# Kernel tuning notes

Hardware: AMD Instinct MI355X
Metric: run time of the kernel (lower is better)

The kernel has to match this reference:

```python
import jax, jax.numpy as jnp
import numpy as np

N_NODES = 100000
N_EDGES = 1600000
D_IN = 64
D_OUT = 64
E_DIM = 32
N_NODE_TYPES = 2
N_EDGE_TYPES = 3


def setup_inputs() -> dict:
    key = jax.random.key(0)
    ks = jax.random.split(key, 7)
    node_feature = jax.random.normal(ks[0], (N_NODES, D_IN), dtype=jnp.float32)
    edge_feature = jax.random.normal(ks[1], (N_EDGES, E_DIM), dtype=jnp.float32)
    # linear_node[i]: Linear(din, dout, bias=False) -> stored as [in, out]
    W_node = jax.random.normal(ks[2], (N_NODE_TYPES, D_IN, D_OUT), dtype=jnp.float32) / np.sqrt(D_IN)
    # linear_msg[i]: Linear(dout + edge_dim, dout, bias=False), msg_direction='single'
    W_msg = jax.random.normal(ks[3], (N_EDGE_TYPES, D_OUT + E_DIM, D_OUT), dtype=jnp.float32) / np.sqrt(D_OUT + E_DIM)
    node_type = jax.random.randint(ks[4], (N_NODES,), 0, N_NODE_TYPES, dtype=jnp.int32)
    edge_type = jax.random.randint(ks[5], (N_EDGES,), 0, N_EDGE_TYPES, dtype=jnp.int32)
    edge_index = jax.random.randint(ks[6], (2, N_EDGES), 0, N_NODES, dtype=jnp.int32)
    return {
        "node_feature": node_feature,
        "edge_feature": edge_feature,
        "W_node": W_node,
        "W_msg": W_msg,
        "node_type": node_type,
        "edge_type": edge_type,
        "edge_index": edge_index,
    }


def reference(node_feature, edge_feature, W_node, W_msg, node_type, edge_type, edge_index):
    # Per-node-type linear: x_out[n] = x[n] @ W_node[node_type[n]]
    # (compute per type, select by mask -- equivalent to masked gather + index_add)
    x_out = jnp.zeros((node_feature.shape[0], W_node.shape[2]), dtype=node_feature.dtype)
    for t in range(W_node.shape[0]):
        x_out = x_out + jnp.where((node_type == t)[:, None],
                                  node_feature @ W_node[t], 0.0)

    src, dst = edge_index[0], edge_index[1]
    # msg_direction == 'single': concat(x_j, edge_feature)  [E, dout+edge_dim]
    x_cat = jnp.concatenate([x_out[src], edge_feature], axis=-1)
    # Per-edge-type linear on messages
    msg = jnp.zeros((x_cat.shape[0], W_msg.shape[2]), dtype=x_cat.dtype)
    for t in range(W_msg.shape[0]):
        msg = msg + jnp.where((edge_type == t)[:, None], x_cat @ W_msg[t], 0.0)

    # normalize_adj=False -> norm is None; aggr='add' scatter into target nodes
    out = jax.ops.segment_sum(msg, dst, num_segments=node_feature.shape[0])
    return out
```

## Files before the change

### kernel.cpp

```cpp
#include <hip/hip_runtime.h>
#include <hip/hip_bf16.h>

#define N_NODES 100000
#define N_EDGES 1600000
#define D_IN 64
#define D_OUT 64
#define E_DIM 32
#define KCAT 288
#define NK (4 * N_NODES)
#define NBCHUNK 391

typedef unsigned long long u64;
typedef __hip_bfloat16 bf16;
typedef unsigned char u8;

__device__ __forceinline__ float bflo(unsigned u) {
    union { unsigned v; float f; } x; x.v = u << 16; return x.f;
}
__device__ __forceinline__ float bfhi(unsigned u) {
    union { unsigned v; float f; } x; x.v = u & 0xffff0000u; return x.f;
}
__device__ __forceinline__ unsigned packbf2(float a, float b) {
    union { bf16 h[2]; unsigned u; } w;
    w.h[0] = __float2bfloat16(a); w.h[1] = __float2bfloat16(b);
    return w.u;
}

__global__ __launch_bounds__(256) void zero_buf(float4* __restrict__ p, long n4) {
    long i = (long)blockIdx.x * 256 + threadIdx.x;
    long stride = (long)gridDim.x * 256;
    float4 z = make_float4(0.f, 0.f, 0.f, 0.f);
    for (; i < n4; i += stride) p[i] = z;
}

__global__ __launch_bounds__(256) void node_xform_g(const float* __restrict__ nf,
                                                    const float* __restrict__ Wn,
                                                    const int* __restrict__ ntype,
                                                    bf16* __restrict__ xout) {
    __shared__ float Ws[2 * 64 * 64];
    __shared__ float As[64][65];
    int tid = threadIdx.x;
    int n0 = blockIdx.x * 64;
    for (int i = tid; i < 2 * 64 * 64; i += 256) Ws[i] = Wn[i];
#pragma unroll
    for (int i = 0; i < 4; ++i) {
        int f = (i * 256 + tid) * 4;
        int r = f >> 6, c = f & 63;
        int n = n0 + r;
        float4 v = (n < N_NODES) ? *(const float4*)&nf[(size_t)n * 64 + c]
                                 : make_float4(0.f, 0.f, 0.f, 0.f);
        As[r][c + 0] = v.x; As[r][c + 1] = v.y; As[r][c + 2] = v.z; As[r][c + 3] = v.w;
    }
    __syncthreads();
    int tx = tid & 15, ty = tid >> 4;
    int r0 = n0 + ty * 4;
    int t0 = (r0 + 0 < N_NODES) ? ntype[r0 + 0] : 0;
    int t1 = (r0 + 1 < N_NODES) ? ntype[r0 + 1] : 0;
    int t2 = (r0 + 2 < N_NODES) ? ntype[r0 + 2] : 0;
    int t3 = (r0 + 3 < N_NODES) ? ntype[r0 + 3] : 0;
    float4 acc0 = {0,0,0,0}, acc1 = {0,0,0,0}, acc2 = {0,0,0,0}, acc3 = {0,0,0,0};
#pragma unroll 8
    for (int k = 0; k < 64; ++k) {
        float4 w0 = *(const float4*)&Ws[k * 64 + tx * 4];
        float4 w1 = *(const float4*)&Ws[4096 + k * 64 + tx * 4];
        float a0 = As[ty * 4 + 0][k];
        float a1 = As[ty * 4 + 1][k];
        float a2 = As[ty * 4 + 2][k];
        float a3 = As[ty * 4 + 3][k];
        float4 wa = t0 ? w1 : w0;
        float4 wb = t1 ? w1 : w0;
        float4 wc = t2 ? w1 : w0;
        float4 wd = t3 ? w1 : w0;
        acc0.x = fmaf(a0, wa.x, acc0.x); acc0.y = fmaf(a0, wa.y, acc0.y);
        acc0.z = fmaf(a0, wa.z, acc0.z); acc0.w = fmaf(a0, wa.w, acc0.w);
        acc1.x = fmaf(a1, wb.x, acc1.x); acc1.y = fmaf(a1, wb.y, acc1.y);
        acc1.z = fmaf(a1, wb.z, acc1.z); acc1.w = fmaf(a1, wb.w, acc1.w);
        acc2.x = fmaf(a2, wc.x, acc2.x); acc2.y = fmaf(a2, wc.y, acc2.y);
        acc2.z = fmaf(a2, wc.z, acc2.z); acc2.w = fmaf(a2, wc.w, acc2.w);
        acc3.x = fmaf(a3, wd.x, acc3.x); acc3.y = fmaf(a3, wd.y, acc3.y);
        acc3.z = fmaf(a3, wd.z, acc3.z); acc3.w = fmaf(a3, wd.w, acc3.w);
    }
#pragma unroll
    for (int r = 0; r < 4; ++r) {
        int n = r0 + r;
        if (n < N_NODES) {
            float4 a = (r == 0) ? acc0 : (r == 1) ? acc1 : (r == 2) ? acc2 : acc3;
            union { bf16 h[4]; uint2 u; } pk;
            pk.h[0] = __float2bfloat16(a.x); pk.h[1] = __float2bfloat16(a.y);
            pk.h[2] = __float2bfloat16(a.z); pk.h[3] = __float2bfloat16(a.w);
            *(uint2*)&xout[(size_t)n * 64 + tx * 4] = pk.u;
        }
    }
}

__global__ __launch_bounds__(256) void count_rank(const int* __restrict__ eidx,
                                                  const int* __restrict__ etype,
                                                  int* __restrict__ cnt,
                                                  u8* __restrict__ rank) {
    int i = blockIdx.x * 256 + threadIdx.x;
    if (i >= N_EDGES / 4) return;
    int4 d = ((const int4*)(eidx + N_EDGES))[i];
    int4 t = ((const int4*)etype)[i];
    int r0 = atomicAdd(&cnt[4 * d.x + t.x], 1);
    int r1 = atomicAdd(&cnt[4 * d.y + t.y], 1);
    int r2 = atomicAdd(&cnt[4 * d.z + t.z], 1);
    int r3 = atomicAdd(&cnt[4 * d.w + t.w], 1);
    ((uchar4*)rank)[i] = make_uchar4((u8)r0, (u8)r1, (u8)r2, (u8)r3);
}

__global__ __launch_bounds__(256) void scan_a(const int* __restrict__ cnt,
                                              int* __restrict__ partials) {
    __shared__ int ws[4];
    int b = blockIdx.x, tid = threadIdx.x, lane = tid & 63, wid = tid >> 6;
    int i0 = b * 1024 + tid * 4;
    int s = 0;
#pragma unroll
    for (int k = 0; k < 4; ++k) { int i = i0 + k; if (i < NK) s += cnt[i]; }
#pragma unroll
    for (int d = 32; d > 0; d >>= 1) s += __shfl_down(s, d);
    if (lane == 0) ws[wid] = s;
    __syncthreads();
    if (tid == 0) partials[b] = ws[0] + ws[1] + ws[2] + ws[3];
}

__global__ __launch_bounds__(512) void scan_b(int* __restrict__ partials) {
    __shared__ int s[512];
    int tid = threadIdx.x;
    int v = (tid < NBCHUNK) ? partials[tid] : 0;
    s[tid] = v;
    __syncthreads();
    for (int d = 1; d < 512; d <<= 1) {
        int u = (tid >= d) ? s[tid - d] : 0;
        __syncthreads();
        s[tid] += u;
        __syncthreads();
    }
    if (tid < NBCHUNK) partials[tid] = s[tid] - v;
}

__global__ __launch_bounds__(256) void scan_c(const int* __restrict__ cnt,
                                              const int* __restrict__ partials,
                                              int* __restrict__ offs) {
    __shared__ int wsum[4];
    int b = blockIdx.x, tid = threadIdx.x, lane = tid & 63, wid = tid >> 6;
    int i0 = b * 1024 + tid * 4;
    int c0 = (i0 + 0 < NK) ? cnt[i0 + 0] : 0;
    int c1 = (i0 + 1 < NK) ? cnt[i0 + 1] : 0;
    int c2 = (i0 + 2 < NK) ? cnt[i0 + 2] : 0;
    int c3 = (i0 + 3 < NK) ? cnt[i0 + 3] : 0;
    int lsum = c0 + c1 + c2 + c3;
    int v = lsum;
#pragma unroll
    for (int d = 1; d < 64; d <<= 1) {
        int u = __shfl_up(v, d);
        if (lane >= d) v += u;
    }
    int wexcl = v - lsum;
    if (lane == 63) wsum[wid] = v;
    __syncthreads();
    int bexcl = 0;
    for (int w = 0; w < wid; ++w) bexcl += wsum[w];
    int base = partials[b] + bexcl + wexcl;
    if (i0 + 0 < NK) offs[i0 + 0] = base; base += c0;
    if (i0 + 1 < NK) offs[i0 + 1] = base; base += c1;
    if (i0 + 2 < NK) offs[i0 + 2] = base; base += c2;
    if (i0 + 3 < NK) offs[i0 + 3] = base;
}

__global__ __launch_bounds__(256) void place_pay(const int* __restrict__ eidx,
                                                 const int* __restrict__ etype,
                                                 const u8* __restrict__ rank,
                                                 const int* __restrict__ offs,
                                                 u64* __restrict__ pay) {
    int i = blockIdx.x * 256 + threadIdx.x;
    if (i >= N_EDGES) return;
    int d = eidx[N_EDGES + i];
    int s = eidx[i];
    int t = etype[i];
    int pos = offs[4 * d + t] + (int)rank[i];
    pay[pos] = (u64)(unsigned)s | ((u64)(unsigned)i << 32);
}

__global__ __launch_bounds__(256) void aggregate_g(const u64* __restrict__ pay,
                                                   const int* __restrict__ offs,
                                                   const bf16* __restrict__ xout,
                                                   const float* __restrict__ ef,
                                                   bf16* __restrict__ B) {
    int wid = threadIdx.x >> 6, lane = threadIdx.x & 63;
    int gw = blockIdx.x * 4 + wid, nw = gridDim.x * 4;
    int c = lane & 31, half = lane >> 5;
    const unsigned short* xo = (const unsigned short*)xout;
    if (gw >= N_NODES) return;

    int4 o = ((const int4*)offs)[gw];
    for (int n = gw; n < N_NODES; n += nw) {
        int nn = n + nw;
        int4 onext;
        if (nn < N_NODES) onext = ((const int4*)offs)[nn];
        int beg = __builtin_amdgcn_readfirstlane(o.x);
        int y   = __builtin_amdgcn_readfirstlane(o.y);
        int z   = __builtin_amdgcn_readfirstlane(o.z);
        int end = __builtin_amdgcn_readfirstlane(o.w);
        float xa0 = 0.f, xa1 = 0.f, xb0 = 0.f, xb1 = 0.f, xc0 = 0.f, xc1 = 0.f;
        float ea = 0.f, eb = 0.f, ec = 0.f;

        for (int base = beg; base < end; base += 64) {
            int m = end - base; if (m > 64) m = 64;
            u64 p = (lane < m) ? pay[base + lane] : 0ull;
            int plo = (int)(unsigned)p;
            int phi = (int)(unsigned)(p >> 32);
            for (int j = 0; j < m; j += 16) {
                int sgp[8], egp[8];
#pragma unroll
                for (int q = 0; q < 8; ++q) {
                    int a  = __builtin_amdgcn_readlane(plo, j + 2 * q);
                    int b2 = __builtin_amdgcn_readlane(plo, j + 2 * q + 1);
                    sgp[q] = half ? b2 : a;
                    a  = __builtin_amdgcn_readlane(phi, j + 2 * q);
                    b2 = __builtin_amdgcn_readlane(phi, j + 2 * q + 1);
                    egp[q] = half ? b2 : a;
                }
                unsigned xv[8];
                float evv[8];
#pragma unroll
                for (int q = 0; q < 8; ++q) {
                    xv[q]  = *(const unsigned*)(xo + (size_t)sgp[q] * 64 + c * 2);
                    evv[q] = ef[(size_t)egp[q] * 32 + c];
                }
#pragma unroll
                for (int q = 0; q < 8; ++q) {
                    float xl = bflo(xv[q]), xh = bfhi(xv[q]);
                    float ev = evv[q];
                    int i0 = base + j + 2 * q;
                    if (i0 + 1 < y) {
                        xa0 += xl; xa1 += xh; ea += ev;
                    } else if (i0 >= y && i0 + 1 < z) {
                        xb0 += xl; xb1 += xh; eb += ev;
                    } else if (i0 >= z && i0 + 1 < end) {
                        xc0 += xl; xc1 += xh; ec += ev;
                    } else {
                        int idx = i0 + half;
                        bool v = idx < end;
                        float fl = v ? xl : 0.f, fh = v ? xh : 0.f, fe = v ? ev : 0.f;
                        if (idx < y)      { xa0 += fl; xa1 += fh; ea += fe; }
                        else if (idx < z) { xb0 += fl; xb1 += fh; eb += fe; }
                        else              { xc0 += fl; xc1 += fh; ec += fe; }
                    }
                }
            }
        }
        xa0 += __shfl_down(xa0, 32); xa1 += __shfl_down(xa1, 32);
        xb0 += __shfl_down(xb0, 32); xb1 += __shfl_down(xb1, 32);
        xc0 += __shfl_down(xc0, 32); xc1 += __shfl_down(xc1, 32);
        ea  += __shfl_down(ea, 32);  eb  += __shfl_down(eb, 32);  ec += __shfl_down(ec, 32);

        if (lane < 32) {
            bf16* Bn = B + (size_t)n * KCAT;
            *(unsigned*)&Bn[2 * c]       = packbf2(xa0, xa1);
            *(unsigned*)&Bn[64 + 2 * c]  = packbf2(xb0, xb1);
            *(unsigned*)&Bn[128 + 2 * c] = packbf2(xc0, xc1);
            Bn[192 + c] = __float2bfloat16(ea);
            Bn[224 + c] = __float2bfloat16(eb);
            Bn[256 + c] = __float2bfloat16(ec);
        }
        o = onext;
    }
}

__global__ __launch_bounds__(256) void final_gemm(const bf16* __restrict__ B,
                                                  const float* __restrict__ Wm,
                                                  float* __restrict__ out) {
    __shared__ float As[64][36];
    __shared__ float Ws[32][64];
    int tid = threadIdx.x;
    int n0 = blockIdx.x * 64;
    int tx = tid & 15;
    int ty = tid >> 4;
    float acc[4][4] = {};

    for (int k0 = 0; k0 < KCAT; k0 += 32) {
        {
            int r = tid >> 2, cb = (tid & 3) * 8;
            int n = n0 + r;
            uint4 v = make_uint4(0u, 0u, 0u, 0u);
            if (n < N_NODES) v = *(const uint4*)&B[(size_t)n * KCAT + k0 + cb];
            *(float4*)&As[r][cb]     = make_float4(bflo(v.x), bfhi(v.x), bflo(v.y), bfhi(v.y));
            *(float4*)&As[r][cb + 4] = make_float4(bflo(v.z), bfhi(v.z), bflo(v.w), bfhi(v.w));
        }
#pragma unroll
        for (int i = 0; i < 2; ++i) {
            int f = (i * 256 + tid) * 4;
            int kk = f >> 6, j = f & 63;
            int r = k0 + kk;
            int t, kin;
            if (r < 192) { t = r >> 6; kin = r & 63; }
            else         { int q = r - 192; t = q >> 5; kin = 64 + (q & 31); }
            *(float4*)&Ws[kk][j] = *(const float4*)&Wm[(t * 96 + kin) * 64 + j];
        }
        __syncthreads();
#pragma unroll
        for (int kk = 0; kk < 32; ++kk) {
            float a0 = As[ty * 4 + 0][kk];
            float a1 = As[ty * 4 + 1][kk];
            float a2 = As[ty * 4 + 2][kk];
            float a3 = As[ty * 4 + 3][kk];
            float4 w = *(const float4*)&Ws[kk][tx * 4];
            acc[0][0] = fmaf(a0, w.x, acc[0][0]); acc[0][1] = fmaf(a0, w.y, acc[0][1]);
            acc[0][2] = fmaf(a0, w.z, acc[0][2]); acc[0][3] = fmaf(a0, w.w, acc[0][3]);
            acc[1][0] = fmaf(a1, w.x, acc[1][0]); acc[1][1] = fmaf(a1, w.y, acc[1][1]);
            acc[1][2] = fmaf(a1, w.z, acc[1][2]); acc[1][3] = fmaf(a1, w.w, acc[1][3]);
            acc[2][0] = fmaf(a2, w.x, acc[2][0]); acc[2][1] = fmaf(a2, w.y, acc[2][1]);
            acc[2][2] = fmaf(a2, w.z, acc[2][2]); acc[2][3] = fmaf(a2, w.w, acc[2][3]);
            acc[3][0] = fmaf(a3, w.x, acc[3][0]); acc[3][1] = fmaf(a3, w.y, acc[3][1]);
            acc[3][2] = fmaf(a3, w.z, acc[3][2]); acc[3][3] = fmaf(a3, w.w, acc[3][3]);
        }
        __syncthreads();
    }
#pragma unroll
    for (int r = 0; r < 4; ++r) {
        int n = n0 + ty * 4 + r;
        if (n < N_NODES) {
            float4 v = make_float4(acc[r][0], acc[r][1], acc[r][2], acc[r][3]);
            *(float4*)&out[(size_t)n * 64 + tx * 4] = v;
        }
    }
}

__global__ __launch_bounds__(256) void fallback_edge(const float* __restrict__ nf,
                                                     const float* __restrict__ ef,
                                                     const float* __restrict__ Wn,
                                                     const float* __restrict__ Wm,
                                                     const int* __restrict__ ntype,
                                                     const int* __restrict__ etype,
                                                     const int* __restrict__ eidx,
                                                     float* __restrict__ out) {
    __shared__ float wn[2 * 64 * 64];
    __shared__ float wm[3 * 96 * 64];
    for (int i = threadIdx.x; i < 2 * 64 * 64; i += 256) wn[i] = Wn[i];
    for (int i = threadIdx.x; i < 3 * 96 * 64; i += 256) wm[i] = Wm[i];
    __syncthreads();
    int wid = threadIdx.x >> 6, lane = threadIdx.x & 63;
    for (int e = blockIdx.x * 4 + wid; e < N_EDGES; e += gridDim.x * 4) {
        int t = etype[e];
        int s = eidx[e];
        int d = eidx[N_EDGES + e];
        int nt = ntype[s];
        float xs = nf[(long)s * 64 + lane];
        const float* wcol = &wn[nt * 4096 + lane];
        float xo = 0.f;
#pragma unroll 16
        for (int k = 0; k < 64; ++k) xo = fmaf(__shfl(xs, k), wcol[k * 64], xo);
        float ev = ef[(long)e * 32 + (lane & 31)];
        const float* mcol = &wm[t * 96 * 64 + lane];
        float m = 0.f;
#pragma unroll 16
        for (int k = 0; k < 64; ++k) m = fmaf(__shfl(xo, k), mcol[k * 64], m);
#pragma unroll 8
        for (int k = 0; k < 32; ++k) m = fmaf(__shfl(ev, k), mcol[(64 + k) * 64], m);
        atomicAdd(&out[(long)d * 64 + lane], m);
    }
}

extern "C" void kernel_launch(void* const* d_in, const int* in_sizes, int n_in,
                              void* d_out, int out_size, void* d_ws, size_t ws_size,
                              hipStream_t stream) {
    const float* nf    = (const float*)d_in[0];
    const float* ef    = (const float*)d_in[1];
    const float* Wn    = (const float*)d_in[2];
    const float* Wm    = (const float*)d_in[3];
    const int*   ntype = (const int*)d_in[4];
    const int*   etype = (const int*)d_in[5];
    const int*   eidx  = (const int*)d_in[6];
    float* out = (float*)d_out;

    const size_t xout_bytes = (size_t)N_NODES * 64 * 2;
    const size_t b_bytes    = (size_t)N_NODES * KCAT * 2;

    if (ws_size >= xout_bytes + b_bytes) {
        bf16* xout = (bf16*)d_ws;
        bf16* B    = (bf16*)((char*)d_ws + xout_bytes);
        u64* pay      = (u64*)d_out;
        int* cnt      = (int*)(pay + N_EDGES);
        int* offs     = cnt + NK;
        int* partials = offs + NK;
        u8*  rank     = (u8*)(partials + 512);

        zero_buf<<<400, 256, 0, stream>>>((float4*)cnt, (long)(NK / 4));
        node_xform_g<<<(N_NODES + 63) / 64, 256, 0, stream>>>(nf, Wn, ntype, xout);
        count_rank<<<(N_EDGES / 4 + 255) / 256, 256, 0, stream>>>(eidx, etype, cnt, rank);
        scan_a<<<NBCHUNK, 256, 0, stream>>>(cnt, partials);
        scan_b<<<1, 512, 0, stream>>>(partials);
        scan_c<<<NBCHUNK, 256, 0, stream>>>(cnt, partials, offs);
        place_pay<<<(N_EDGES + 255) / 256, 256, 0, stream>>>(eidx, etype, rank, offs, pay);
        aggregate_g<<<4096, 256, 0, stream>>>(pay, offs, xout, ef, B);
        final_gemm<<<(N_NODES + 63) / 64, 256, 0, stream>>>(B, Wm, out);
    } else {
        zero_buf<<<2048, 256, 0, stream>>>((float4*)d_out, (long)((size_t)out_size * 4 / 16));
        fallback_edge<<<4096, 256, 0, stream>>>(nf, ef, Wn, Wm, ntype, etype, eidx, out);
    }
}
```

Baseline: 310.6 us.

## Fuse count zeroing into node transform and prefetch next node's payload in aggregation

Removes the separate zero_buf launch by zeroing the count array inside node_xform_g. count_rank is switched to one edge per thread with scalar loads. aggregate_g now loads the first payload chunk of the next node while processing the current node, to hide memory latency. The single-edge count_rank loses int4 vectorized loads and adds more threads.

```diff
diff --git a/kernel.cpp b/kernel.cpp
--- a/kernel.cpp
+++ b/kernel.cpp
@@ -36,11 +36,16 @@
 __global__ __launch_bounds__(256) void node_xform_g(const float* __restrict__ nf,
                                                     const float* __restrict__ Wn,
                                                     const int* __restrict__ ntype,
-                                                    bf16* __restrict__ xout) {
+                                                    bf16* __restrict__ xout,
+                                                    int* __restrict__ cnt) {
     __shared__ float Ws[2 * 64 * 64];
     __shared__ float As[64][65];
     int tid = threadIdx.x;
     int n0 = blockIdx.x * 64;
+    {
+        int zi = blockIdx.x * 256 + tid;
+        if (zi < NK) cnt[zi] = 0;
+    }
     for (int i = tid; i < 2 * 64 * 64; i += 256) Ws[i] = Wn[i];
 #pragma unroll
     for (int i = 0; i < 4; ++i) {
@@ -98,14 +103,11 @@
                                                   int* __restrict__ cnt,
                                                   u8* __restrict__ rank) {
     int i = blockIdx.x * 256 + threadIdx.x;
-    if (i >= N_EDGES / 4) return;
-    int4 d = ((const int4*)(eidx + N_EDGES))[i];
-    int4 t = ((const int4*)etype)[i];
-    int r0 = atomicAdd(&cnt[4 * d.x + t.x], 1);
-    int r1 = atomicAdd(&cnt[4 * d.y + t.y], 1);
-    int r2 = atomicAdd(&cnt[4 * d.z + t.z], 1);
-    int r3 = atomicAdd(&cnt[4 * d.w + t.w], 1);
-    ((uchar4*)rank)[i] = make_uchar4((u8)r0, (u8)r1, (u8)r2, (u8)r3);
+    if (i >= N_EDGES) return;
+    int d = eidx[N_EDGES + i];
+    int t = etype[i];
+    int r = atomicAdd(&cnt[4 * d + t], 1);
+    rank[i] = (u8)r;
 }
 
 __global__ __launch_bounds__(256) void scan_a(const int* __restrict__ cnt,
@@ -193,10 +195,28 @@
     if (gw >= N_NODES) return;
 
     int4 o = ((const int4*)offs)[gw];
+    {
+        int b0 = __builtin_amdgcn_readfirstlane(o.x);
+        int e0 = __builtin_amdgcn_readfirstlane(o.w);
+        (void)b0; (void)e0;
+    }
+    u64 p = 0ull;
+    {
+        int beg = __builtin_amdgcn_readfirstlane(o.x);
+        int end = __builtin_amdgcn_readfirstlane(o.w);
+        if (beg + lane < end) p = pay[beg + lane];
+    }
+
     for (int n = gw; n < N_NODES; n += nw) {
         int nn = n + nw;
-        int4 onext;
-        if (nn < N_NODES) onext = ((const int4*)offs)[nn];
+        int4 onext = make_int4(0, 0, 0, 0);
+        u64 pnext = 0ull;
+        if (nn < N_NODES) {
+            onext = ((const int4*)offs)[nn];
+            int nbeg = __builtin_amdgcn_readfirstlane(onext.x);
+            int nend = __builtin_amdgcn_readfirstlane(onext.w);
+            if (nbeg + lane < nend) pnext = pay[nbeg + lane];
+        }
         int beg = __builtin_amdgcn_readfirstlane(o.x);
         int y   = __builtin_amdgcn_readfirstlane(o.y);
         int z   = __builtin_amdgcn_readfirstlane(o.z);
@@ -204,11 +224,12 @@
         float xa0 = 0.f, xa1 = 0.f, xb0 = 0.f, xb1 = 0.f, xc0 = 0.f, xc1 = 0.f;
         float ea = 0.f, eb = 0.f, ec = 0.f;
 
+        u64 pcur = p;
         for (int base = beg; base < end; base += 64) {
             int m = end - base; if (m > 64) m = 64;
-            u64 p = (lane < m) ? pay[base + lane] : 0ull;
-            int plo = (int)(unsigned)p;
-            int phi = (int)(unsigned)(p >> 32);
+            if (base != beg) pcur = (lane < m) ? pay[base + lane] : 0ull;
+            int plo = (int)(unsigned)pcur;
+            int phi = (int)(unsigned)(pcur >> 32);
             for (int j = 0; j < m; j += 16) {
                 int sgp[8], egp[8];
 #pragma unroll
@@ -264,6 +285,7 @@
             Bn[256 + c] = __float2bfloat16(ec);
         }
         o = onext;
+        p = pnext;
     }
 }
 
@@ -385,9 +407,8 @@
         int* partials = offs + NK;
         u8*  rank     = (u8*)(partials + 512);
 
-        zero_buf<<<400, 256, 0, stream>>>((float4*)cnt, (long)(NK / 4));
-        node_xform_g<<<(N_NODES + 63) / 64, 256, 0, stream>>>(nf, Wn, ntype, xout);
-        count_rank<<<(N_EDGES / 4 + 255) / 256, 256, 0, stream>>>(eidx, etype, cnt, rank);
+        node_xform_g<<<(N_NODES + 63) / 64, 256, 0, stream>>>(nf, Wn, ntype, xout, cnt);
+        count_rank<<<(N_EDGES + 255) / 256, 256, 0, stream>>>(eidx, etype, cnt, rank);
         scan_a<<<NBCHUNK, 256, 0, stream>>>(cnt, partials);
         scan_b<<<1, 512, 0, stream>>>(partials);
         scan_c<<<NBCHUNK, 256, 0, stream>>>(cnt, partials, offs);
```

New measurement: 307.8 us. Within noise of the previous version (-0.9%).
